# Optimization experiments

Hardware: AMD Instinct MI355X
Metric: run time of the kernel (lower is better)

Reference implementation:

```python
import jax, jax.numpy as jnp
import numpy as np
from jax import lax

N = 131072

# ---- soft logic gates on {0,1}-valued floats ----
def XOR(a, b): return a + b - 2.0 * a * b
def AND(a, b): return a * b
def OR(a, b):  return a + b - a * b
def NOT(a):    return 1.0 - a
def MUX(sel, a, b):  # sel==1 -> a, sel==0 -> b
    return sel * a + (1.0 - sel) * b
def and_tree(x): return jnp.prod(x, axis=-1, keepdims=True)
def or_tree(x):  return 1.0 - jnp.prod(1.0 - x, axis=-1, keepdims=True)

def ripple_sub(a, b):
    """a - b on LSB-first bit vectors [..., n]; returns (diff_bits, borrow_out [...,1])."""
    at = jnp.moveaxis(a, -1, 0)
    bt = jnp.moveaxis(b, -1, 0)
    def step(borrow, ab):
        ai, bi = ab
        axb = XOR(ai, bi)
        d = XOR(axb, borrow)
        bout = OR(AND(NOT(ai), bi), AND(NOT(axb), borrow))
        return bout, d
    b0 = jnp.zeros(a.shape[:-1], a.dtype)
    bout, d = lax.scan(step, b0, (at, bt))
    return jnp.moveaxis(d, 0, -1), bout[..., None]

def ripple_add(a, b):
    """a + b on LSB-first bit vectors [..., n]; returns (sum_bits, carry_out [...,1])."""
    at = jnp.moveaxis(a, -1, 0)
    bt = jnp.moveaxis(b, -1, 0)
    def step(c, ab):
        ai, bi = ab
        axb = XOR(ai, bi)
        s = XOR(axb, c)
        cout = OR(AND(ai, bi), AND(axb, c))
        return cout, s
    c0 = jnp.zeros(a.shape[:-1], a.dtype)
    cout, s = lax.scan(step, c0, (at, bt))
    return jnp.moveaxis(s, 0, -1), cout[..., None]

def div_iteration(R_lsb, D_lsb):
    """Restoring division step. R,D LSB-first [...,55]. Returns (q_bit [...,1], R_next_lsb)."""
    R_trial, borrow = ripple_sub(R_lsb, D_lsb)
    q = NOT(borrow)
    R_next = MUX(borrow, R_lsb, R_trial)
    return q, R_next

def _forward(A, B):
    A, B = jnp.broadcast_arrays(A, B)
    bs = A.shape[:-1]
    dt = A.dtype
    z1 = jnp.zeros(bs + (1,), dt)
    o1 = jnp.ones(bs + (1,), dt)

    s_a, e_a, m_a = A[..., 0:1], A[..., 1:12], A[..., 12:64]
    s_b, e_b, m_b = B[..., 0:1], B[..., 1:12], B[..., 12:64]

    s_out = XOR(s_a, s_b)

    # ---- special-case detection ----
    e_a_all_one, e_b_all_one = and_tree(e_a), and_tree(e_b)
    e_a_is_zero, e_b_is_zero = NOT(or_tree(e_a)), NOT(or_tree(e_b))
    m_a_any, m_b_any = or_tree(m_a), or_tree(m_b)
    m_a_is_zero, m_b_is_zero = NOT(m_a_any), NOT(m_b_any)
    a_is_zero = AND(e_a_is_zero, m_a_is_zero)
    b_is_zero = AND(e_b_is_zero, m_b_is_zero)
    a_is_inf = AND(e_a_all_one, m_a_is_zero)
    b_is_inf = AND(e_b_all_one, m_b_is_zero)
    a_is_nan = AND(e_a_all_one, m_a_any)
    b_is_nan = AND(e_b_all_one, m_b_any)
    either_nan = OR(a_is_nan, b_is_nan)
    div_by_zero = AND(NOT(a_is_zero), b_is_zero)
    zero_div_zero = AND(a_is_zero, b_is_zero)
    inf_div_inf = AND(a_is_inf, b_is_inf)
    result_is_nan = OR(either_nan, OR(zero_div_zero, inf_div_inf))
    inf_div_y = AND(a_is_inf, NOT(b_is_inf))
    result_is_inf = OR(div_by_zero, inf_div_y)
    zero_div_x = AND(a_is_zero, NOT(b_is_zero))
    x_div_inf = AND(NOT(a_is_inf), b_is_inf)
    result_is_zero = OR(zero_div_x, x_div_inf)

    # ---- exponent: e_a - e_b + 1023 (13-bit LSB-first) ----
    e_a_13 = jnp.concatenate([e_a[..., ::-1], z1, z1], axis=-1)
    e_b_13 = jnp.concatenate([e_b[..., ::-1], z1, z1], axis=-1)
    exp_diff, _ = ripple_sub(e_a_13, e_b_13)
    const_1023 = jnp.concatenate([o1] * 10 + [z1] * 3, axis=-1)
    exp_result, _ = ripple_add(exp_diff, const_1023)

    # ---- 57-step restoring division of 55-bit mantissas (MSB-first registers) ----
    A_55 = jnp.concatenate([z1, o1, m_a, z1], axis=-1)  # [0 | 1.m_a | 0]
    D_55 = jnp.concatenate([z1, o1, m_b, z1], axis=-1)
    D_lsb = D_55[..., ::-1]

    def div_step(R, _):
        q, R_sub_lsb = div_iteration(R[..., ::-1], D_lsb)
        R_sub = R_sub_lsb[..., ::-1]
        R_next = jnp.concatenate([R_sub[..., 1:], z1], axis=-1)  # shift left
        return R_next, q[..., 0]

    R_carry, qs = lax.scan(div_step, A_55, jnp.arange(56))
    q_last, R_last_lsb = div_iteration(R_carry[..., ::-1], D_lsb)
    R = R_last_lsb[..., ::-1]
    Q_raw = jnp.concatenate([jnp.moveaxis(qs, 0, -1), q_last], axis=-1)  # [...,57]

    # ---- normalize + RNE rounding ----
    q0 = Q_raw[..., 0:1]
    need_normalize = NOT(q0)
    remainder_nonzero = or_tree(R)
    mant_normal = Q_raw[..., 1:53]
    round_normal = Q_raw[..., 53:54]
    sticky_normal = or_tree(jnp.concatenate([Q_raw[..., 54:57], remainder_nonzero], axis=-1))
    mant_shifted = Q_raw[..., 2:54]
    round_shifted = Q_raw[..., 54:55]
    sticky_shifted = or_tree(jnp.concatenate([Q_raw[..., 55:57], remainder_nonzero], axis=-1))
    mant_52 = MUX(q0, mant_normal, mant_shifted)
    round_bit = MUX(q0, round_normal, round_shifted)
    sticky_bit = MUX(q0, sticky_normal, sticky_shifted)

    const_1_13 = jnp.concatenate([o1] + [z1] * 12, axis=-1)
    exp_minus1, _ = ripple_sub(exp_result, const_1_13)
    exp_adjusted = MUX(need_normalize, exp_minus1, exp_result)

    lsb = mant_52[..., -1:]
    round_up = AND(round_bit, OR(sticky_bit, lsb))
    mant_53_lsb = jnp.concatenate([mant_52[..., ::-1], z1], axis=-1)
    round_inc_lsb = jnp.concatenate([round_up] + [z1] * 52, axis=-1)
    mant_rounded_lsb, carry = ripple_add(mant_53_lsb, round_inc_lsb)
    mant_final = mant_rounded_lsb[..., :52][..., ::-1]

    exp_plus1, _ = ripple_add(exp_adjusted, const_1_13)
    exp_final_13 = MUX(carry, exp_plus1, exp_adjusted)
    zero_52 = jnp.zeros(bs + (52,), dt)
    mant_final = MUX(carry, zero_52, mant_final)

    exp_final = exp_final_13[..., :11][..., ::-1]
    is_overflow = or_tree(exp_final_13[..., 11:13])
    exp_is_zero = NOT(or_tree(exp_final_13))
    exp_sign = exp_final_13[..., 12:13]
    is_underflow = OR(exp_sign, exp_is_zero)

    result = jnp.concatenate([s_out, exp_final, mant_final], axis=-1)

    # ---- special-value muxes ----
    ones11 = jnp.ones(bs + (11,), dt)
    nan_mant = jnp.concatenate([o1] + [z1] * 51, axis=-1)
    nan_val = jnp.concatenate([s_out, ones11, nan_mant], axis=-1)
    inf_val = jnp.concatenate([s_out, ones11, zero_52], axis=-1)
    zero_val = jnp.concatenate([s_out, jnp.zeros(bs + (11,), dt), zero_52], axis=-1)

    result = MUX(result_is_nan, nan_val, result)
    not_nan = NOT(result_is_nan)
    is_inf_valid = AND(result_is_inf, not_nan)
    result = MUX(is_inf_valid, inf_val, result)
    not_inf = NOT(result_is_inf)
    is_zero_valid = AND(result_is_zero, AND(not_nan, not_inf))
    result = MUX(is_zero_valid, zero_val, result)
    overflow_valid = AND(is_overflow, AND(not_nan, AND(not_inf, NOT(result_is_zero))))
    result = MUX(overflow_valid, inf_val, result)
    underflow_valid = AND(is_underflow, AND(not_nan, AND(not_inf, AND(NOT(is_overflow), NOT(result_is_zero)))))
    result = MUX(underflow_valid, zero_val, result)
    return result


def setup_inputs() -> dict:
    key = jax.random.key(0)
    kA, kB = jax.random.split(key)
    A = jax.random.randint(kA, (N, 64), 0, 2).astype(jnp.float32)
    B = jax.random.randint(kB, (N, 64), 0, 2).astype(jnp.float32)
    return {"A": A, "B": B}


def reference(A, B):
    return _forward(A, B)
```

## Files before the change

kernel.cpp:

```cpp
#include <hip/hip_runtime.h>
#include <stdint.h>

#define M52 0xFFFFFFFFFFFFFULL

__device__ __forceinline__ uint64_t shfl64(uint64_t x, int src) {
    int lo = __shfl((int)(uint32_t)x, src, 64);
    int hi = __shfl((int)(uint32_t)(x >> 32), src, 64);
    return ((uint64_t)(uint32_t)hi << 32) | (uint64_t)(uint32_t)lo;
}

__global__ __launch_bounds__(256, 2) void fp64div_kernel(
    const float* __restrict__ A, const float* __restrict__ B,
    float* __restrict__ out, int n_rows)
{
    const int tid  = blockIdx.x * blockDim.x + threadIdx.x;
    const int lane = threadIdx.x & 63;
    const int wave_base = tid & ~63;
    if (wave_base >= n_rows) return;

    const float* Ap = A + (size_t)wave_base * 64 + lane;
    const float* Bp = B + (size_t)wave_base * 64 + lane;

    float fa0[32], fa1[32], fb0[32], fb1[32];
    uint64_t my_a = 0, my_b = 0;

    #pragma unroll
    for (int r = 0; r < 32; ++r) fa0[r] = Ap[(size_t)r * 64];
    #pragma unroll
    for (int r = 0; r < 32; ++r) fb0[r] = Bp[(size_t)r * 64];

    #pragma unroll
    for (int r = 0; r < 32; ++r) {
        uint64_t m = __ballot(fa0[r] != 0.0f);
        if (lane == r) my_a = m;
    }
    #pragma unroll
    for (int r = 0; r < 32; ++r) fa1[r] = Ap[(size_t)(r + 32) * 64];

    #pragma unroll
    for (int r = 0; r < 32; ++r) {
        uint64_t m = __ballot(fb0[r] != 0.0f);
        if (lane == r) my_b = m;
    }
    #pragma unroll
    for (int r = 0; r < 32; ++r) fb1[r] = Bp[(size_t)(r + 32) * 64];

    #pragma unroll
    for (int r = 0; r < 32; ++r) {
        uint64_t m = __ballot(fa1[r] != 0.0f);
        if (lane == r + 32) my_a = m;
    }
    #pragma unroll
    for (int r = 0; r < 32; ++r) {
        uint64_t m = __ballot(fb1[r] != 0.0f);
        if (lane == r + 32) my_b = m;
    }

    const uint64_t av = __brevll(my_a);
    const uint64_t bv = __brevll(my_b);

    const uint32_t sa = (uint32_t)(av >> 63), sb = (uint32_t)(bv >> 63);
    const uint32_t s_out = sa ^ sb;
    const uint32_t Ea = (uint32_t)(av >> 52) & 0x7FFu;
    const uint32_t Eb = (uint32_t)(bv >> 52) & 0x7FFu;
    const uint64_t Ma = av & M52;
    const uint64_t Mb = bv & M52;

    const bool ea_all1 = (Ea == 0x7FFu), eb_all1 = (Eb == 0x7FFu);
    const bool ea_zero = (Ea == 0u),     eb_zero = (Eb == 0u);
    const bool ma_zero = (Ma == 0ull),   mb_zero = (Mb == 0ull);
    const bool a_zero = ea_zero && ma_zero, b_zero = eb_zero && mb_zero;
    const bool a_inf  = ea_all1 && ma_zero, b_inf  = eb_all1 && mb_zero;
    const bool a_nan  = ea_all1 && !ma_zero, b_nan = eb_all1 && !mb_zero;

    const bool r_nan  = a_nan || b_nan || (a_zero && b_zero) || (a_inf && b_inf);
    const bool r_inf  = (!a_zero && b_zero) || (a_inf && !b_inf);
    const bool r_zero = (a_zero && !b_zero) || (!a_inf && b_inf);

    const uint32_t exp13 = (Ea - Eb + 1023u) & 0x1FFFu;

    uint64_t R = (1ULL << 53) | (Ma << 1);
    const uint64_t D = (1ULL << 53) | (Mb << 1);
    uint64_t Q = 0;
    #pragma unroll
    for (int i = 0; i < 56; ++i) {
        const bool ge = (R >= D);
        const uint64_t t = R - D;
        R = ge ? t : R;
        Q = (Q << 1) | (ge ? 1u : 0u);
        R <<= 1;
    }
    {
        const bool ge = (R >= D);
        const uint64_t t = R - D;
        R = ge ? t : R;
        Q = (Q << 1) | (ge ? 1u : 0u);
    }

    const uint32_t q0 = (uint32_t)(Q >> 56) & 1u;
    const uint32_t rem_nz = (R != 0ull) ? 1u : 0u;

    const uint64_t mant52 = q0 ? ((Q >> 4) & M52) : ((Q >> 3) & M52);
    const uint32_t rbit   = q0 ? ((uint32_t)(Q >> 3) & 1u) : ((uint32_t)(Q >> 2) & 1u);
    const uint32_t sticky = (q0 ? (((Q & 7ull) != 0ull) ? 1u : 0u)
                                : (((Q & 3ull) != 0ull) ? 1u : 0u)) | rem_nz;
    const uint32_t exp_f  = q0 ? exp13 : ((exp13 - 1u) & 0x1FFFu);

    const uint32_t lsb = (uint32_t)mant52 & 1u;
    const uint32_t rup = rbit & (sticky | lsb);
    const uint64_t mant_final = (mant52 + rup) & M52;

    const uint32_t exp11   = exp_f & 0x7FFu;
    const bool overflow  = (exp_f >> 11) != 0u;
    const bool underflow = (((exp_f >> 12) & 1u) != 0u) || (exp_f == 0u);

    uint64_t res = ((uint64_t)s_out << 63) | ((uint64_t)exp11 << 52) | mant_final;
    const uint64_t zero_v = ((uint64_t)s_out << 63);
    const uint64_t inf_v  = zero_v | (0x7FFULL << 52);
    const uint64_t nan_v  = inf_v | (1ULL << 51);

    if (r_nan)          res = nan_v;
    else if (r_inf)     res = inf_v;
    else if (r_zero)    res = zero_v;
    else if (overflow)  res = inf_v;
    else if (underflow) res = zero_v;

    const uint64_t out_word = __brevll(res);

    float* Op = out + (size_t)wave_base * 64 + lane;
    #pragma unroll
    for (int r = 0; r < 64; ++r) {
        const uint64_t w = shfl64(out_word, r);
        Op[(size_t)r * 64] = (float)((uint32_t)(w >> lane) & 1u);
    }
}

extern "C" void kernel_launch(void* const* d_in, const int* in_sizes, int n_in,
                              void* d_out, int out_size, void* d_ws, size_t ws_size,
                              hipStream_t stream) {
    const float* A = (const float*)d_in[0];
    const float* B = (const float*)d_in[1];
    float* out = (float*)d_out;
    const int n_rows = in_sizes[0] / 64;
    const int threads = 256;
    const int blocks = (n_rows + threads - 1) / threads;
    fp64div_kernel<<<blocks, threads, 0, stream>>>(A, B, out, n_rows);
}
```

Before: 99.88 us.

## Process two row chunks per wave, prefetching the second while computing the first

Each wave now handles two 64-row chunks, one from each half of the input. It loads the second chunk's A and B bits while it converts, divides and stores the first chunk. The goal is to overlap memory latency with the divide and shuffle-store work, and to halve the grid. The cost is 128 live floats of registers per thread, so launch bounds drop to one block per SIMD, which cuts occupancy. The kernel assumes an even row count.

```diff
diff --git a/kernel.cpp b/kernel.cpp
--- a/kernel.cpp
+++ b/kernel.cpp
@@ -9,58 +9,11 @@
     return ((uint64_t)(uint32_t)hi << 32) | (uint64_t)(uint32_t)lo;
 }
 
-__global__ __launch_bounds__(256, 2) void fp64div_kernel(
-    const float* __restrict__ A, const float* __restrict__ B,
-    float* __restrict__ out, int n_rows)
-{
-    const int tid  = blockIdx.x * blockDim.x + threadIdx.x;
-    const int lane = threadIdx.x & 63;
-    const int wave_base = tid & ~63;
-    if (wave_base >= n_rows) return;
+__device__ __forceinline__ uint64_t circuit_divide(uint64_t pa, uint64_t pb) {
+    const uint64_t av = __brevll(pa);
+    const uint64_t bv = __brevll(pb);
 
-    const float* Ap = A + (size_t)wave_base * 64 + lane;
-    const float* Bp = B + (size_t)wave_base * 64 + lane;
-
-    float fa0[32], fa1[32], fb0[32], fb1[32];
-    uint64_t my_a = 0, my_b = 0;
-
-    #pragma unroll
-    for (int r = 0; r < 32; ++r) fa0[r] = Ap[(size_t)r * 64];
-    #pragma unroll
-    for (int r = 0; r < 32; ++r) fb0[r] = Bp[(size_t)r * 64];
-
-    #pragma unroll
-    for (int r = 0; r < 32; ++r) {
-        uint64_t m = __ballot(fa0[r] != 0.0f);
-        if (lane == r) my_a = m;
-    }
-    #pragma unroll
-    for (int r = 0; r < 32; ++r) fa1[r] = Ap[(size_t)(r + 32) * 64];
-
-    #pragma unroll
-    for (int r = 0; r < 32; ++r) {
-        uint64_t m = __ballot(fb0[r] != 0.0f);
-        if (lane == r) my_b = m;
-    }
-    #pragma unroll
-    for (int r = 0; r < 32; ++r) fb1[r] = Bp[(size_t)(r + 32) * 64];
-
-    #pragma unroll
-    for (int r = 0; r < 32; ++r) {
-        uint64_t m = __ballot(fa1[r] != 0.0f);
-        if (lane == r + 32) my_a = m;
-    }
-    #pragma unroll
-    for (int r = 0; r < 32; ++r) {
-        uint64_t m = __ballot(fb1[r] != 0.0f);
-        if (lane == r + 32) my_b = m;
-    }
-
-    const uint64_t av = __brevll(my_a);
-    const uint64_t bv = __brevll(my_b);
-
-    const uint32_t sa = (uint32_t)(av >> 63), sb = (uint32_t)(bv >> 63);
-    const uint32_t s_out = sa ^ sb;
+    const uint32_t s_out = (uint32_t)((av ^ bv) >> 63);
     const uint32_t Ea = (uint32_t)(av >> 52) & 0x7FFu;
     const uint32_t Eb = (uint32_t)(bv >> 52) & 0x7FFu;
     const uint64_t Ma = av & M52;
@@ -125,13 +78,74 @@
     else if (overflow)  res = inf_v;
     else if (underflow) res = zero_v;
 
-    const uint64_t out_word = __brevll(res);
+    return __brevll(res);
+}
 
-    float* Op = out + (size_t)wave_base * 64 + lane;
+__global__ __launch_bounds__(256, 1) void fp64div_kernel(
+    const float* __restrict__ A, const float* __restrict__ B,
+    float* __restrict__ out, int half_rows)
+{
+    const int tid  = blockIdx.x * blockDim.x + threadIdx.x;
+    const int lane = threadIdx.x & 63;
+    const int wb   = tid & ~63;
+    if (wb >= half_rows) return;
+
+    const size_t off0 = (size_t)wb * 64 + lane;
+    const size_t off1 = off0 + (size_t)half_rows * 64;
+    const float* Ap0 = A + off0;
+    const float* Bp0 = B + off0;
+    const float* Ap1 = A + off1;
+    const float* Bp1 = B + off1;
+
+    float fa[64], fb[64];
+
+    #pragma unroll
+    for (int r = 0; r < 64; ++r) fa[r] = Ap0[(size_t)r * 64];
+    #pragma unroll
+    for (int r = 0; r < 64; ++r) fb[r] = Bp0[(size_t)r * 64];
+
+    uint64_t a0 = 0, b0 = 0;
     #pragma unroll
     for (int r = 0; r < 64; ++r) {
-        const uint64_t w = shfl64(out_word, r);
-        Op[(size_t)r * 64] = (float)((uint32_t)(w >> lane) & 1u);
+        uint64_t m = __ballot(fa[r] != 0.0f);
+        if (lane == r) a0 = m;
+    }
+    #pragma unroll
+    for (int r = 0; r < 64; ++r) fa[r] = Ap1[(size_t)r * 64];
+
+    #pragma unroll
+    for (int r = 0; r < 64; ++r) {
+        uint64_t m = __ballot(fb[r] != 0.0f);
+        if (lane == r) b0 = m;
+    }
+    #pragma unroll
+    for (int r = 0; r < 64; ++r) fb[r] = Bp1[(size_t)r * 64];
+
+    const uint64_t w0 = circuit_divide(a0, b0);
+    float* Op0 = out + off0;
+    #pragma unroll
+    for (int r = 0; r < 64; ++r) {
+        const uint64_t w = shfl64(w0, r);
+        Op0[(size_t)r * 64] = (float)((uint32_t)(w >> lane) & 1u);
+    }
+
+    uint64_t a1 = 0, b1 = 0;
+    #pragma unroll
+    for (int r = 0; r < 64; ++r) {
+        uint64_t m = __ballot(fa[r] != 0.0f);
+        if (lane == r) a1 = m;
+    }
+    #pragma unroll
+    for (int r = 0; r < 64; ++r) {
+        uint64_t m = __ballot(fb[r] != 0.0f);
+        if (lane == r) b1 = m;
+    }
+    const uint64_t w1 = circuit_divide(a1, b1);
+    float* Op1 = out + off1;
+    #pragma unroll
+    for (int r = 0; r < 64; ++r) {
+        const uint64_t w = shfl64(w1, r);
+        Op1[(size_t)r * 64] = (float)((uint32_t)(w >> lane) & 1u);
     }
 }
 
@@ -142,7 +156,8 @@
     const float* B = (const float*)d_in[1];
     float* out = (float*)d_out;
     const int n_rows = in_sizes[0] / 64;
+    const int half = n_rows >> 1;
     const int threads = 256;
-    const int blocks = (n_rows + threads - 1) / threads;
-    fp64div_kernel<<<blocks, threads, 0, stream>>>(A, B, out, n_rows);
+    const int blocks = (half + threads - 1) / threads;
+    fp64div_kernel<<<blocks, threads, 0, stream>>>(A, B, out, half);
 }
```

New measurement: 103.3 us. 1.03x slower.
